# Kernel tuning notes

Measured on AMD Instinct MI355X. Metric: run time of the kernel, lower is better.

Reference implementation:

```python
import jax, jax.numpy as jnp
import numpy as np

N = 50000   # num nodes
D = 64      # feature dim
E = 800000  # num edges (avg degree 16)


def setup_inputs() -> dict:
    key = jax.random.key(0)
    k1, k2, k3 = jax.random.split(key, 3)
    x = jax.random.normal(k1, (N, D), dtype=jnp.float32)
    edge_index = jax.random.randint(k2, (2, E), 0, N, dtype=jnp.int32)
    edge_weight = jax.random.uniform(k3, (E,), dtype=jnp.float32)
    return {"x": x, "edge_index": edge_index, "edge_weight": edge_weight}


def reference(x, edge_index, edge_weight):
    """Faithful translation of scatter_median (spmm with reduce='median'):
    per destination node, the (lower) median over its weighted incoming
    neighbor messages, computed independently per feature channel.
    Nodes with zero in-degree produce zeros (as in the torch code where
    h is initialized to zeros and degree-0 rows are skipped).
    """
    n, d = x.shape
    e = edge_index.shape[1]

    # sort edges by destination (stable sort; within-segment order is irrelevant for median)
    order = jnp.argsort(edge_index[1])
    row = edge_index[0, order]
    col = edge_index[1, order]
    w = edge_weight[order]

    # weighted messages: x_j = x[row] * w  -> [E, D]
    x_j = x[row] * w[:, None]

    # per-destination degree and position of each edge within its segment
    deg = jnp.bincount(col, length=n)                                   # [N]
    starts = jnp.concatenate([jnp.zeros(1, deg.dtype), jnp.cumsum(deg)[:-1]])
    pos = jnp.arange(e, dtype=deg.dtype) - starts[col]                  # [E]

    # dense batch [N, max_deg, D], padded with +inf so pads sort to the end
    max_deg = int(jnp.max(deg))  # concrete on materialized inputs
    dense = jnp.full((n, max_deg, d), jnp.inf, dtype=x.dtype)
    dense = dense.at[col, pos].set(x_j)

    # per-channel sort, then pick the lower-median index (torch.median semantics:
    # for even counts it returns the lower of the two middle values)
    dense = jnp.sort(dense, axis=1)
    idx = jnp.maximum((deg - 1) // 2, 0)                                # [N]
    med = jnp.take_along_axis(dense, idx[:, None, None], axis=1)[:, 0]  # [N, D]

    return jnp.where(deg[:, None] > 0, med, jnp.zeros((), dtype=x.dtype))
```

## Files before the change

kernel.cpp:

```cpp
#include <hip/hip_runtime.h>
#include <stdint.h>
#include <math.h>

#define NN 50000
#define DD 64
#define EE 800000
#define BSZ 64
#define NB 782
#define BCAP 1280
#define EPW 4096
#define CAP 48
#define BIGMAX 1024


__global__ void zero_cnt(int* __restrict__ cnt) {
    int i = blockIdx.x * blockDim.x + threadIdx.x;
    if (i < NB + 1) cnt[i] = 0;
}

__global__ __launch_bounds__(512) void bucketize(
        const int* __restrict__ ei, const float* __restrict__ ew,
        int* __restrict__ bucket_cnt, uint64_t* __restrict__ recs) {
    __shared__ uint64_t       srt[EPW];
    __shared__ unsigned short bktS[EPW];
    __shared__ int hist[NB];
    __shared__ int off[NB];
    __shared__ int base[NB];
    const int t  = threadIdx.x;
    const int e0 = blockIdx.x * EPW;
    const int nE = (e0 + EPW < EE) ? EPW : (EE - e0);

    for (int i = t; i < NB; i += 512) hist[i] = 0;
    __syncthreads();

    for (int i = t; i < nE; i += 512)
        atomicAdd(&hist[ei[EE + e0 + i] >> 6], 1);
    __syncthreads();

    if (t < 64) {
        int loc[13];
        int s = 0;
        #pragma unroll
        for (int k = 0; k < 13; ++k) {
            int i = t * 13 + k;
            int h = (i < NB) ? hist[i] : 0;
            loc[k] = s;
            s += h;
        }
        const int tot = s;
        int run = tot;
        #pragma unroll
        for (int d = 1; d < 64; d <<= 1) {
            int v = __shfl_up(run, d, 64);
            if (t >= d) run += v;
        }
        const int basex = run - tot;
        #pragma unroll
        for (int k = 0; k < 13; ++k) {
            int i = t * 13 + k;
            if (i < NB) off[i] = basex + loc[k];
        }
    }
    __syncthreads();

    for (int i = t; i < NB; i += 512) {
        int c = hist[i];
        base[i] = (c > 0) ? atomicAdd(&bucket_cnt[i], c) : 0;
    }
    __syncthreads();
    for (int i = t; i < NB; i += 512) hist[i] = 0;
    __syncthreads();

    for (int i = t; i < nE; i += 512) {
        int   s = ei[e0 + i];
        int   d = ei[EE + e0 + i];
        float w = ew[e0 + i];
        int   b = d >> 6;
        int   p = atomicAdd(&hist[b], 1);
        int idx = off[b] + p;
        srt[idx]  = ((uint64_t)__float_as_uint(w) << 32) |
                    ((uint32_t)s << 6) | (uint32_t)(d & 63);
        bktS[idx] = (unsigned short)b;
    }
    __syncthreads();

    for (int i = t; i < nE; i += 512) {
        uint64_t r = srt[i];
        int b   = bktS[i];
        int pos = base[b] + (i - off[b]);
        if (pos < BCAP)
            recs[(size_t)b * BCAP + pos] = r;
    }
}

__global__ __launch_bounds__(256) void bin_dense(
        const int* __restrict__ bucket_cnt, const uint64_t* __restrict__ recs,
        uint64_t* __restrict__ slots, int* __restrict__ deg,
        int* __restrict__ big_cnt, int* __restrict__ big_list) {
    __shared__ __align__(16) uint64_t sl[BSZ * CAP];
    __shared__ int degl[BSZ];
    const int t = threadIdx.x;
    const int b = blockIdx.x;

    int cnt = bucket_cnt[b];
    if (cnt > BCAP) cnt = BCAP;

    for (int i = t; i < BSZ; i += 256) degl[i] = 0;
    __syncthreads();

    const uint64_t* br = recs + (size_t)b * BCAP;
    for (int i = t; i < cnt; i += 256) {
        uint64_t r = br[i];
        int loc = (int)(r & 63u);
        int p = atomicAdd(&degl[loc], 1);
        if (p < CAP)
            sl[loc * CAP + p] = (r & 0xFFFFFFFF00000000ull)
                              | (uint32_t)(((uint32_t)r) >> 6);
    }
    __syncthreads();

    ulonglong2*       o2 = (ulonglong2*)(slots + (size_t)b * BSZ * CAP);
    const ulonglong2* s2 = (const ulonglong2*)sl;
    for (int i = t; i < BSZ * CAP / 2; i += 256) o2[i] = s2[i];
    int n0 = b * BSZ;
    for (int i = t; i < BSZ; i += 256) {
        int n = n0 + i;
        if (n < NN) {
            int dgi = degl[i];
            if (dgi > CAP) dgi = CAP;
            deg[n] = dgi;
            if (dgi > 32) {
                int q = atomicAdd(big_cnt, 1);
                if (q < BIGMAX) big_list[q] = n;
            }
        }
    }
}

__device__ __forceinline__ void cswap(int& a, int& b) {
    int lo = min(a, b);
    int hi = max(a, b);
    a = lo; b = hi;
}

template<int I, int END, int R, int STEP, int AW>
struct Pairs {
    static __device__ __forceinline__ void run(int (&r)[AW]) {
        if constexpr (I + R < END) {
            cswap(r[I], r[I + R]);
            Pairs<I + STEP, END, R, STEP, AW>::run(r);
        }
    }
};

template<int LO, int N, int R, int AW>
struct Merge {
    static __device__ __forceinline__ void run(int (&r)[AW]) {
        if constexpr (2 * R < N) {
            Merge<LO,     N, 2 * R, AW>::run(r);
            Merge<LO + R, N, 2 * R, AW>::run(r);
            Pairs<LO + R, LO + N, R, 2 * R, AW>::run(r);
        } else {
            cswap(r[LO], r[LO + R]);
        }
    }
};

template<int LO, int N, int AW>
struct Sorter {
    static __device__ __forceinline__ void run(int (&r)[AW]) {
        if constexpr (N > 1) {
            Sorter<LO,         N / 2, AW>::run(r);
            Sorter<LO + N / 2, N / 2, AW>::run(r);
            Merge<LO, N, 1, AW>::run(r);
        }
    }
};

__device__ __forceinline__ int f2key(float f) {
    int s = __float_as_int(f);
    return s ^ ((s >> 31) & 0x7fffffff);
}
__device__ __forceinline__ float key2f(int kk) {
    return __int_as_float(kk ^ ((kk >> 31) & 0x7fffffff));
}

template <int PW, int REAL, int KLO, int KHI>
__device__ __forceinline__ float gather_sort_u(const float* __restrict__ x, int lane,
                                               int dg, int k,
                                               const uint64_t* __restrict__ row) {
    int r[PW];
    #pragma unroll
    for (int j = 0; j < PW; ++j) {
        int kj;
        if (j < REAL) {
            float v = INFINITY;
            if (j < dg) {
                uint64_t s = row[j];
                uint32_t src = (uint32_t)(s & 0xffffffffu);
                float    w   = __uint_as_float((uint32_t)(s >> 32));
                v = x[(size_t)src * DD + lane] * w;
            }
            kj = f2key(v);
        } else {
            kj = 0x7fffffff;
        }
        r[j] = kj;
    }
    Sorter<0, PW, PW>::run(r);
    int med = r[KLO];
    #pragma unroll
    for (int t = KLO + 1; t <= KHI; ++t)
        if (t == k) med = r[t];
    return key2f(med);
}

__global__ __launch_bounds__(256, 4) void median_main(
    const float* __restrict__ x, const int* __restrict__ deg,
    const uint64_t* __restrict__ slots, float* __restrict__ out) {
    const int lane = threadIdx.x & 63;
    const int wid  = (blockIdx.x * blockDim.x + threadIdx.x) >> 6;
    const int S    = (gridDim.x * blockDim.x) >> 6;

    for (int n0 = wid; n0 < NN; n0 += S) {
        const int n = __builtin_amdgcn_readfirstlane(n0);
        int dg = __builtin_amdgcn_readfirstlane(deg[n]);
        if (dg > 32) continue;

        float med = 0.f;
        if (dg > 0) {
            const uint64_t* row = slots + (size_t)n * CAP;
            const int k = (dg - 1) >> 1;
            if      (dg <= 2)  med = gather_sort_u< 2,  2,  0,  0>(x, lane, dg, k, row);
            else if (dg <= 4)  med = gather_sort_u< 4,  4,  1,  1>(x, lane, dg, k, row);
            else if (dg <= 8)  med = gather_sort_u< 8,  8,  2,  3>(x, lane, dg, k, row);
            else if (dg <= 12) med = gather_sort_u<16, 12,  4,  5>(x, lane, dg, k, row);
            else if (dg <= 16) med = gather_sort_u<16, 16,  6,  7>(x, lane, dg, k, row);
            else if (dg <= 20) med = gather_sort_u<32, 20,  8,  9>(x, lane, dg, k, row);
            else if (dg <= 24) med = gather_sort_u<32, 24, 10, 11>(x, lane, dg, k, row);
            else               med = gather_sort_u<32, 32, 12, 15>(x, lane, dg, k, row);
        }
        out[(size_t)n * DD + lane] = med;
    }
}

__global__ __launch_bounds__(256) void median_big(
    const float* __restrict__ x, const int* __restrict__ deg,
    const uint64_t* __restrict__ slots, const int* __restrict__ big_cnt,
    const int* __restrict__ big_list, float* __restrict__ out) {
    const int lane = threadIdx.x & 63;
    const int wid  = (blockIdx.x * blockDim.x + threadIdx.x) >> 6;
    const int S    = (gridDim.x * blockDim.x) >> 6;

    int cnt = __builtin_amdgcn_readfirstlane(big_cnt[0]);
    if (cnt > BIGMAX) cnt = BIGMAX;

    for (int i = wid; i < cnt; i += S) {
        int n  = __builtin_amdgcn_readfirstlane(big_list[i]);
        int dg = __builtin_amdgcn_readfirstlane(deg[n]);
        const uint64_t* row = slots + (size_t)n * CAP;
        int r[64];
        #pragma unroll
        for (int j = 0; j < 64; ++j) {
            int kj;
            if (j < CAP) {
                float v = INFINITY;
                if (j < dg) {
                    uint64_t s = row[j];
                    uint32_t src = (uint32_t)(s & 0xffffffffu);
                    float    w   = __uint_as_float((uint32_t)(s >> 32));
                    v = x[(size_t)src * DD + lane] * w;
                }
                kj = f2key(v);
            } else {
                kj = 0x7fffffff;
            }
            r[j] = kj;
        }
        Sorter<0, 64, 64>::run(r);
        const int k = (dg - 1) >> 1;
        int med = r[16];
        #pragma unroll
        for (int t = 17; t <= 23; ++t)
            if (t == k) med = r[t];
        out[(size_t)n * DD + lane] = key2f(med);
    }
}

extern "C" void kernel_launch(void* const* d_in, const int* in_sizes, int n_in,
                              void* d_out, int out_size, void* d_ws, size_t ws_size,
                              hipStream_t stream) {
    const float*  x  = (const float*)d_in[0];
    const int*    ei = (const int*)d_in[1];
    const float*  ew = (const float*)d_in[2];
    float* out = (float*)d_out;

    int*      bucket_cnt = (int*)d_ws;
    int*      big_cnt    = bucket_cnt + NB;
    int*      big_list   = (int*)((char*)d_ws + (1 << 12));
    int*      deg        = (int*)((char*)d_ws + (1 << 14));
    uint64_t* recs       = (uint64_t*)((char*)d_ws + (1 << 18));
    uint64_t* slots      = (uint64_t*)((char*)d_ws + (1 << 23));

    zero_cnt<<<(NB + 1 + 255) / 256, 256, 0, stream>>>(bucket_cnt);
    bucketize<<<(EE + EPW - 1) / EPW, 512, 0, stream>>>(ei, ew, bucket_cnt, recs);
    bin_dense<<<NB, 256, 0, stream>>>(bucket_cnt, recs, slots, deg, big_cnt, big_list);
    median_main<<<2048, 256, 0, stream>>>(x, deg, slots, out);
    median_big<<<16, 256, 0, stream>>>(x, deg, slots, big_cnt, big_list, out);
}
```

Before: 133.6 us.

## Fuse binning and median into one kernel reading neighbor slots from LDS

Merges the bin_dense and median_main kernels so each block bins its 64 destination nodes into shared memory and then computes the medians directly from LDS. This removes the global write and re-read of the dense slots array and the degree array, plus one kernel launch. High-degree nodes get their slots copied into a compact big_slots buffer, with the degree packed into big_list. Per-edge source and weight are now read via readfirstlane as scalars. Parallelism drops to 782 blocks of 512 threads, and shared-memory use of about 24KB per block may limit occupancy.

```diff
diff --git a/kernel.cpp b/kernel.cpp
--- a/kernel.cpp
+++ b/kernel.cpp
@@ -93,50 +93,6 @@
     }
 }
 
-__global__ __launch_bounds__(256) void bin_dense(
-        const int* __restrict__ bucket_cnt, const uint64_t* __restrict__ recs,
-        uint64_t* __restrict__ slots, int* __restrict__ deg,
-        int* __restrict__ big_cnt, int* __restrict__ big_list) {
-    __shared__ __align__(16) uint64_t sl[BSZ * CAP];
-    __shared__ int degl[BSZ];
-    const int t = threadIdx.x;
-    const int b = blockIdx.x;
-
-    int cnt = bucket_cnt[b];
-    if (cnt > BCAP) cnt = BCAP;
-
-    for (int i = t; i < BSZ; i += 256) degl[i] = 0;
-    __syncthreads();
-
-    const uint64_t* br = recs + (size_t)b * BCAP;
-    for (int i = t; i < cnt; i += 256) {
-        uint64_t r = br[i];
-        int loc = (int)(r & 63u);
-        int p = atomicAdd(&degl[loc], 1);
-        if (p < CAP)
-            sl[loc * CAP + p] = (r & 0xFFFFFFFF00000000ull)
-                              | (uint32_t)(((uint32_t)r) >> 6);
-    }
-    __syncthreads();
-
-    ulonglong2*       o2 = (ulonglong2*)(slots + (size_t)b * BSZ * CAP);
-    const ulonglong2* s2 = (const ulonglong2*)sl;
-    for (int i = t; i < BSZ * CAP / 2; i += 256) o2[i] = s2[i];
-    int n0 = b * BSZ;
-    for (int i = t; i < BSZ; i += 256) {
-        int n = n0 + i;
-        if (n < NN) {
-            int dgi = degl[i];
-            if (dgi > CAP) dgi = CAP;
-            deg[n] = dgi;
-            if (dgi > 32) {
-                int q = atomicAdd(big_cnt, 1);
-                if (q < BIGMAX) big_list[q] = n;
-            }
-        }
-    }
-}
-
 __device__ __forceinline__ void cswap(int& a, int& b) {
     int lo = min(a, b);
     int hi = max(a, b);
@@ -186,7 +142,7 @@
 }
 
 template <int PW, int REAL, int KLO, int KHI>
-__device__ __forceinline__ float gather_sort_u(const float* __restrict__ x, int lane,
+__device__ __forceinline__ float gather_sort_l(const float* __restrict__ x, int lane,
                                                int dg, int k,
                                                const uint64_t* __restrict__ row) {
     int r[PW];
@@ -197,9 +153,10 @@
             float v = INFINITY;
             if (j < dg) {
                 uint64_t s = row[j];
-                uint32_t src = (uint32_t)(s & 0xffffffffu);
-                float    w   = __uint_as_float((uint32_t)(s >> 32));
-                v = x[(size_t)src * DD + lane] * w;
+                int src = __builtin_amdgcn_readfirstlane((int)(uint32_t)(s & 0xffffffffu));
+                int wb  = __builtin_amdgcn_readfirstlane((int)(uint32_t)(s >> 32));
+                float w = __uint_as_float((uint32_t)wb);
+                v = x[(size_t)(uint32_t)src * DD + lane] * w;
             }
             kj = f2key(v);
         } else {
@@ -215,63 +172,103 @@
     return key2f(med);
 }
 
-__global__ __launch_bounds__(256, 4) void median_main(
-    const float* __restrict__ x, const int* __restrict__ deg,
-    const uint64_t* __restrict__ slots, float* __restrict__ out) {
+__global__ __launch_bounds__(512) void bin_median(
+        const float* __restrict__ x, const int* __restrict__ bucket_cnt,
+        const uint64_t* __restrict__ recs, uint64_t* __restrict__ big_slots,
+        int* __restrict__ big_cnt, int* __restrict__ big_list,
+        float* __restrict__ out) {
+    __shared__ __align__(16) uint64_t sl[BSZ * CAP];
+    __shared__ int degl[BSZ];
+    const int t = threadIdx.x;
+    const int b = blockIdx.x;
+
+    int cnt = bucket_cnt[b];
+    if (cnt > BCAP) cnt = BCAP;
+
+    for (int i = t; i < BSZ; i += 512) degl[i] = 0;
+    __syncthreads();
+
+    const uint64_t* br = recs + (size_t)b * BCAP;
+    for (int i = t; i < cnt; i += 512) {
+        uint64_t r = br[i];
+        int loc = (int)(r & 63u);
+        int p = atomicAdd(&degl[loc], 1);
+        if (p < CAP)
+            sl[loc * CAP + p] = (r & 0xFFFFFFFF00000000ull)
+                              | (uint32_t)(((uint32_t)r) >> 6);
+    }
+    __syncthreads();
+
+    if (t < BSZ) {
+        int dgi = degl[t];
+        if (dgi > CAP) dgi = CAP;
+        int n = b * BSZ + t;
+        if (dgi > 32 && n < NN) {
+            int q = atomicAdd(big_cnt, 1);
+            if (q < BIGMAX) {
+                big_list[q] = (n << 6) | dgi;
+                for (int j = 0; j < CAP; ++j)
+                    big_slots[(size_t)q * CAP + j] = sl[t * CAP + j];
+            }
+        }
+    }
+
+    const int lane = t & 63;
+    const int wv   = t >> 6;
+    for (int loc = wv; loc < BSZ; loc += 8) {
+        int n = b * BSZ + loc;
+        if (n >= NN) break;
+
+        int dg = __builtin_amdgcn_readfirstlane(degl[loc]);
+        if (dg > CAP) dg = CAP;
+        if (dg > 32) continue;
+
+        float med = 0.f;
+        if (dg > 0) {
+            const uint64_t* row = &sl[loc * CAP];
+            const int k = (dg - 1) >> 1;
+            if      (dg <= 2)  med = gather_sort_l< 2,  2,  0,  0>(x, lane, dg, k, row);
+            else if (dg <= 4)  med = gather_sort_l< 4,  4,  1,  1>(x, lane, dg, k, row);
+            else if (dg <= 8)  med = gather_sort_l< 8,  8,  2,  3>(x, lane, dg, k, row);
+            else if (dg <= 12) med = gather_sort_l<16, 12,  4,  5>(x, lane, dg, k, row);
+            else if (dg <= 16) med = gather_sort_l<16, 16,  6,  7>(x, lane, dg, k, row);
+            else if (dg <= 20) med = gather_sort_l<32, 20,  8,  9>(x, lane, dg, k, row);
+            else if (dg <= 24) med = gather_sort_l<32, 24, 10, 11>(x, lane, dg, k, row);
+            else               med = gather_sort_l<32, 32, 12, 15>(x, lane, dg, k, row);
+        }
+        out[(size_t)n * DD + lane] = med;
+    }
+}
+
+__global__ __launch_bounds__(256) void median_big(
+    const float* __restrict__ x, const uint64_t* __restrict__ big_slots,
+    const int* __restrict__ big_cnt, const int* __restrict__ big_list,
+    float* __restrict__ out) {
     const int lane = threadIdx.x & 63;
     const int wid  = (blockIdx.x * blockDim.x + threadIdx.x) >> 6;
     const int S    = (gridDim.x * blockDim.x) >> 6;
 
-    for (int n0 = wid; n0 < NN; n0 += S) {
-        const int n = __builtin_amdgcn_readfirstlane(n0);
-        int dg = __builtin_amdgcn_readfirstlane(deg[n]);
-        if (dg > 32) continue;
-
-        float med = 0.f;
-        if (dg > 0) {
-            const uint64_t* row = slots + (size_t)n * CAP;
-            const int k = (dg - 1) >> 1;
-            if      (dg <= 2)  med = gather_sort_u< 2,  2,  0,  0>(x, lane, dg, k, row);
-            else if (dg <= 4)  med = gather_sort_u< 4,  4,  1,  1>(x, lane, dg, k, row);
-            else if (dg <= 8)  med = gather_sort_u< 8,  8,  2,  3>(x, lane, dg, k, row);
-            else if (dg <= 12) med = gather_sort_u<16, 12,  4,  5>(x, lane, dg, k, row);
-            else if (dg <= 16) med = gather_sort_u<16, 16,  6,  7>(x, lane, dg, k, row);
-            else if (dg <= 20) med = gather_sort_u<32, 20,  8,  9>(x, lane, dg, k, row);
-            else if (dg <= 24) med = gather_sort_u<32, 24, 10, 11>(x, lane, dg, k, row);
-            else               med = gather_sort_u<32, 32, 12, 15>(x, lane, dg, k, row);
-        }
-        out[(size_t)n * DD + lane] = med;
-    }
-}
-
-__global__ __launch_bounds__(256) void median_big(
-    const float* __restrict__ x, const int* __restrict__ deg,
-    const uint64_t* __restrict__ slots, const int* __restrict__ big_cnt,
-    const int* __restrict__ big_list, float* __restrict__ out) {
-    const int lane = threadIdx.x & 63;
-    const int wid  = (blockIdx.x * blockDim.x + threadIdx.x) >> 6;
-    const int S    = (gridDim.x * blockDim.x) >> 6;
-
     int cnt = __builtin_amdgcn_readfirstlane(big_cnt[0]);
     if (cnt > BIGMAX) cnt = BIGMAX;
 
     for (int i = wid; i < cnt; i += S) {
-        int n  = __builtin_amdgcn_readfirstlane(big_list[i]);
-        int dg = __builtin_amdgcn_readfirstlane(deg[n]);
-        const uint64_t* row = slots + (size_t)n * CAP;
+        int v  = __builtin_amdgcn_readfirstlane(big_list[i]);
+        int n  = v >> 6;
+        int dg = v & 63;
+        const uint64_t* row = big_slots + (size_t)i * CAP;
         int r[64];
         #pragma unroll
         for (int j = 0; j < 64; ++j) {
             int kj;
             if (j < CAP) {
-                float v = INFINITY;
+                float vv = INFINITY;
                 if (j < dg) {
                     uint64_t s = row[j];
                     uint32_t src = (uint32_t)(s & 0xffffffffu);
                     float    w   = __uint_as_float((uint32_t)(s >> 32));
-                    v = x[(size_t)src * DD + lane] * w;
+                    vv = x[(size_t)src * DD + lane] * w;
                 }
-                kj = f2key(v);
+                kj = f2key(vv);
             } else {
                 kj = 0x7fffffff;
             }
@@ -298,13 +295,12 @@
     int*      bucket_cnt = (int*)d_ws;
     int*      big_cnt    = bucket_cnt + NB;
     int*      big_list   = (int*)((char*)d_ws + (1 << 12));
-    int*      deg        = (int*)((char*)d_ws + (1 << 14));
     uint64_t* recs       = (uint64_t*)((char*)d_ws + (1 << 18));
-    uint64_t* slots      = (uint64_t*)((char*)d_ws + (1 << 23));
+    uint64_t* big_slots  = (uint64_t*)((char*)d_ws + (1 << 23));
 
     zero_cnt<<<(NB + 1 + 255) / 256, 256, 0, stream>>>(bucket_cnt);
     bucketize<<<(EE + EPW - 1) / EPW, 512, 0, stream>>>(ei, ew, bucket_cnt, recs);
-    bin_dense<<<NB, 256, 0, stream>>>(bucket_cnt, recs, slots, deg, big_cnt, big_list);
-    median_main<<<2048, 256, 0, stream>>>(x, deg, slots, out);
-    median_big<<<16, 256, 0, stream>>>(x, deg, slots, big_cnt, big_list, out);
-}
+    bin_median<<<NB, 512, 0, stream>>>(x, bucket_cnt, recs, big_slots,
+                                       big_cnt, big_list, out);
+    median_big<<<16, 256, 0, stream>>>(x, big_slots, big_cnt, big_list, out);
+}
```

Result: no change. 134.2 us (+0.5%).
